# Optimization experiments

Hardware: AMD Instinct MI355X
Metric: run time of the kernel (lower is better)

The kernel has to match this reference:

```python
import jax, jax.numpy as jnp
import numpy as np

N, E, D, L, G = 50000, 625000, 128, 3, 64
EPS = 1e-5


def setup_inputs() -> dict:
    key = jax.random.key(0)
    ks = jax.random.split(key, 16)
    s = 1.0 / np.sqrt(D)
    inp = {
        "x": jax.random.normal(ks[0], (N, D), jnp.float32),
        "edge_index": jax.random.randint(ks[1], (2, E), 0, N, jnp.int64),
        "batch": jnp.sort(jax.random.randint(ks[2], (N,), 0, G, jnp.int64)),
        # node_emb
        "Wemb": jax.random.normal(ks[3], (D, D), jnp.float32) * s,
        "bemb": jnp.zeros((D,), jnp.float32),
        # per-layer params stacked on axis 0
        "Wscore": jax.random.normal(ks[4], (L, 1, D), jnp.float32) * s,
        "bscore": jnp.zeros((L, 1), jnp.float32),
        "Wfwd": jax.random.normal(ks[5], (L, D, D), jnp.float32) * s,
        "Wbwd": jax.random.normal(ks[6], (L, D, D), jnp.float32) * s,
        "Wself": jax.random.normal(ks[7], (L, D, D), jnp.float32) * s,
        "bself": jnp.zeros((L, D), jnp.float32),
        "Wcomb": jax.random.normal(ks[8], (L, D, 3 * D), jnp.float32) * s,
        "bcomb": jnp.zeros((L, D), jnp.float32),
        "gamma": jnp.ones((L, D), jnp.float32),
        "beta": jnp.zeros((L, D), jnp.float32),
    }
    return inp


def reference(x, edge_index, batch, Wemb, bemb, Wscore, bscore, Wfwd, Wbwd,
              Wself, bself, Wcomb, bcomb, gamma, beta):
    n = x.shape[0]
    src, dst = edge_index[0], edge_index[1]  # j (source), i (target)
    h = jax.nn.relu(x @ Wemb.T + bemb)       # dropout is eval-mode no-op
    for l in range(Wscore.shape[0]):
        identity = h
        scores = h @ Wscore[l].T + bscore[l]           # [N, 1]
        h_fwd = h @ Wfwd[l].T                          # [N, D]
        h_bwd = h @ Wbwd[l].T
        h_self = h @ Wself[l].T + bself[l]
        alpha = jax.nn.sigmoid(scores[src] - scores[dst])  # [E, 1]
        aggr_fwd = jax.ops.segment_sum(h_fwd[src] * alpha, dst, num_segments=n)
        aggr_bwd = jax.ops.segment_sum(h_bwd[src] * (1.0 - alpha), dst, num_segments=n)
        z = jnp.concatenate([h_self, aggr_fwd, aggr_bwd], axis=-1) @ Wcomb[l].T + bcomb[l]
        mu = jnp.mean(z, axis=-1, keepdims=True)
        var = jnp.var(z, axis=-1, keepdims=True)
        z = (z - mu) * jax.lax.rsqrt(var + EPS) * gamma[l] + beta[l]
        h = jax.nn.relu(z) + identity
    # global mean pool over graphs
    sums = jax.ops.segment_sum(h, batch, num_segments=G)
    cnt = jax.ops.segment_sum(jnp.ones((n,), h.dtype), batch, num_segments=G)
    return sums / jnp.maximum(cnt, 1.0)[:, None]
```

## Files before the change

### kernel.cpp

```cpp
#include <hip/hip_runtime.h>
#include <math.h>

#define EPS 1e-5f
#define PS 8
#define SW(row) (((row) & 7) << 4)

typedef __attribute__((ext_vector_type(8))) short short8;
typedef __attribute__((ext_vector_type(4))) float f32x4;

__device__ __forceinline__ float bf2f(unsigned short u) {
  union { unsigned i; float f; } c; c.i = ((unsigned)u) << 16; return c.f;
}
__device__ __forceinline__ float bflo(unsigned u) {
  union { unsigned i; float f; } c; c.i = u << 16; return c.f;
}
__device__ __forceinline__ float bfhi(unsigned u) {
  union { unsigned i; float f; } c; c.i = u & 0xFFFF0000u; return c.f;
}
__device__ __forceinline__ unsigned short f2bf(float f) {
  union { float f; unsigned i; } c; c.f = f;
  unsigned r = c.i + 0x7FFF + ((c.i >> 16) & 1);
  return (unsigned short)(r >> 16);
}

template <bool SCORE>
__global__ __launch_bounds__(256, 2) void embed_gemm(
    const float* __restrict__ X,
    const ushort* __restrict__ W,
    const float* __restrict__ bias,
    const float* __restrict__ Wsc, const float* __restrict__ bsc,
    ushort* __restrict__ hb, float* __restrict__ scores, int M) {
  __shared__ __align__(16) ushort As[64 * 128];
  __shared__ __align__(16) ushort Ws[128 * 128];
  __shared__ float lds3[64][2];

  const int t = threadIdx.x;
  const int lane = t & 63;
  const int w = t >> 6;
  const int wm = w >> 1, wn = w & 1;
  const int m0 = blockIdx.x * 64;
  const int l15 = lane & 15, l16 = lane >> 4;

  short8 ar[4], wr_[8];
#pragma unroll
  for (int it = 0; it < 4; ++it) {
    int chunk = it * 256 + t;
    int row = chunk >> 4;
    int b16 = chunk & 15;
    int grow = m0 + row; if (grow >= M) grow = M - 1;
    const float* xr = X + (size_t)grow * 128 + b16 * 8;
    float4 f0 = *(const float4*)xr;
    float4 f1 = *(const float4*)(xr + 4);
    short8 v;
    v[0] = (short)f2bf(f0.x); v[1] = (short)f2bf(f0.y);
    v[2] = (short)f2bf(f0.z); v[3] = (short)f2bf(f0.w);
    v[4] = (short)f2bf(f1.x); v[5] = (short)f2bf(f1.y);
    v[6] = (short)f2bf(f1.z); v[7] = (short)f2bf(f1.w);
    ar[it] = v;
  }
#pragma unroll
  for (int it = 0; it < 8; ++it) {
    int chunk = it * 256 + t;
    int row = chunk >> 4;
    int b16 = chunk & 15;
    wr_[it] = *(const short8*)(W + (size_t)row * 128 + b16 * 8);
  }
#pragma unroll
  for (int it = 0; it < 4; ++it) {
    int chunk = it * 256 + t;
    int row = chunk >> 4, b = (chunk & 15) * 16;
    *(short8*)((char*)As + row * 256 + (b ^ SW(row))) = ar[it];
  }
#pragma unroll
  for (int it = 0; it < 8; ++it) {
    int chunk = it * 256 + t;
    int row = chunk >> 4, b = (chunk & 15) * 16;
    *(short8*)((char*)Ws + row * 256 + (b ^ SW(row))) = wr_[it];
  }
  __syncthreads();

  f32x4 acc[2][4];
#pragma unroll
  for (int i = 0; i < 2; ++i)
#pragma unroll
    for (int j = 0; j < 4; ++j) acc[i][j] = (f32x4){0.f, 0.f, 0.f, 0.f};

#pragma unroll
  for (int kk = 0; kk < 4; ++kk) {
    int cb = kk * 64 + l16 * 16;
    short8 a[2], b[4];
#pragma unroll
    for (int i = 0; i < 2; ++i) {
      int row = wm * 32 + i * 16 + l15;
      a[i] = *(const short8*)((const char*)As + row * 256 + (cb ^ SW(row)));
    }
#pragma unroll
    for (int j = 0; j < 4; ++j) {
      int row = wn * 64 + j * 16 + l15;
      b[j] = *(const short8*)((const char*)Ws + row * 256 + (cb ^ SW(row)));
    }
#pragma unroll
    for (int i = 0; i < 2; ++i)
#pragma unroll
      for (int j = 0; j < 4; ++j)
        acc[i][j] = __builtin_amdgcn_mfma_f32_16x16x32_bf16(a[i], b[j], acc[i][j], 0, 0, 0);
  }

#pragma unroll
  for (int i = 0; i < 2; ++i)
#pragma unroll
    for (int r = 0; r < 4; ++r) {
      int row = m0 + wm * 32 + i * 16 + l16 * 4 + r;
      bool valid = row < M;
      float psc = 0.f;
#pragma unroll
      for (int j = 0; j < 4; ++j) {
        int colw = wn * 64 + j * 16 + l15;
        float v = acc[i][j][r] + bias[colw];
        v = fmaxf(v, 0.f);
        if (valid) hb[(size_t)row * 128 + colw] = f2bf(v);
        if (SCORE) psc += v * Wsc[colw];
      }
      if (SCORE) {
#pragma unroll
        for (int mm = 1; mm <= 8; mm <<= 1) psc += __shfl_xor(psc, mm, 64);
        if (l15 == 0) lds3[wm * 32 + i * 16 + l16 * 4 + r][wn] = psc;
      }
    }
  if (SCORE) {
    __syncthreads();
    if (wn == 0 && l15 == 0) {
#pragma unroll
      for (int i = 0; i < 2; ++i)
#pragma unroll
        for (int r = 0; r < 4; ++r) {
          int rl = wm * 32 + i * 16 + l16 * 4 + r;
          int row = blockIdx.x * 64 + rl;
          if (row < M) scores[row] = lds3[rl][0] + lds3[rl][1] + bsc[0];
        }
    }
  }
}

template <bool SCORE>
__global__ __launch_bounds__(256, 2) void layer_gemm(
    const ushort* __restrict__ A0,
    const ushort* __restrict__ A1,
    const ushort* __restrict__ W,
    const float* __restrict__ bias,
    const float* __restrict__ gamma, const float* __restrict__ beta,
    const float* __restrict__ Wsc, const float* __restrict__ bsc,
    ushort* __restrict__ hb, float* __restrict__ scores, int M) {
  __shared__ __align__(16) ushort As[64 * 192];
  __shared__ __align__(16) ushort Ws[128 * 192];
  __shared__ float lds1[64][2];
  __shared__ float lds2[64][2];
  __shared__ float lds3[64][2];

  const int t = threadIdx.x;
  const int lane = t & 63;
  const int w = t >> 6;
  const int wm = w >> 1, wn = w & 1;
  const int m0 = blockIdx.x * 64;
  const int l15 = lane & 15, l16 = lane >> 4;

  f32x4 acc[2][4];
#pragma unroll
  for (int i = 0; i < 2; ++i)
#pragma unroll
    for (int j = 0; j < 4; ++j) acc[i][j] = (f32x4){0.f, 0.f, 0.f, 0.f};

#pragma unroll
  for (int hf = 0; hf < 2; ++hf) {
    short8 ar[6], wr_[12];
#pragma unroll
    for (int it = 0; it < 6; ++it) {
      int chunk = it * 256 + t;
      int row = chunk / 24;
      int b16 = chunk % 24;
      int ec = hf * 192 + b16 * 8;
      int grow = m0 + row; if (grow >= M) grow = M - 1;
      const ushort* src = (ec < 128) ? (A0 + (size_t)grow * 128 + ec)
                                     : (A1 + (size_t)grow * 256 + (ec - 128));
      ar[it] = *(const short8*)src;
    }
#pragma unroll
    for (int it = 0; it < 12; ++it) {
      int chunk = it * 256 + t;
      int row = chunk / 24;
      int b16 = chunk % 24;
      wr_[it] = *(const short8*)(W + (size_t)row * 384 + hf * 192 + b16 * 8);
    }
    __syncthreads();
#pragma unroll
    for (int it = 0; it < 6; ++it) {
      int chunk = it * 256 + t;
      int row = chunk / 24, b = (chunk % 24) * 16;
      *(short8*)((char*)As + row * 384 + (b ^ SW(row))) = ar[it];
    }
#pragma unroll
    for (int it = 0; it < 12; ++it) {
      int chunk = it * 256 + t;
      int row = chunk / 24, b = (chunk % 24) * 16;
      *(short8*)((char*)Ws + row * 384 + (b ^ SW(row))) = wr_[it];
    }
    __syncthreads();
#pragma unroll
    for (int kk = 0; kk < 6; ++kk) {
      int cb = kk * 64 + l16 * 16;
      short8 a[2], b[4];
#pragma unroll
      for (int i = 0; i < 2; ++i) {
        int row = wm * 32 + i * 16 + l15;
        a[i] = *(const short8*)((const char*)As + row * 384 + (cb ^ SW(row)));
      }
#pragma unroll
      for (int j = 0; j < 4; ++j) {
        int row = wn * 64 + j * 16 + l15;
        b[j] = *(const short8*)((const char*)Ws + row * 384 + (cb ^ SW(row)));
      }
#pragma unroll
      for (int i = 0; i < 2; ++i)
#pragma unroll
        for (int j = 0; j < 4; ++j)
          acc[i][j] = __builtin_amdgcn_mfma_f32_16x16x32_bf16(a[i], b[j], acc[i][j], 0, 0, 0);
    }
  }

#pragma unroll
  for (int i = 0; i < 2; ++i)
#pragma unroll
    for (int r = 0; r < 4; ++r) {
      float p1 = 0.f, p2 = 0.f;
#pragma unroll
      for (int j = 0; j < 4; ++j) {
        int colw = wn * 64 + j * 16 + l15;
        float v = acc[i][j][r] + bias[colw];
        acc[i][j][r] = v;
        p1 += v;
        p2 += v * v;
      }
#pragma unroll
      for (int mm = 1; mm <= 8; mm <<= 1) {
        p1 += __shfl_xor(p1, mm, 64);
        p2 += __shfl_xor(p2, mm, 64);
      }
      if (l15 == 0) {
        int rl = wm * 32 + i * 16 + l16 * 4 + r;
        lds1[rl][wn] = p1;
        lds2[rl][wn] = p2;
      }
    }
  __syncthreads();
#pragma unroll
  for (int i = 0; i < 2; ++i)
#pragma unroll
    for (int r = 0; r < 4; ++r) {
      int rl = wm * 32 + i * 16 + l16 * 4 + r;
      int row = m0 + rl;
      bool valid = row < M;
      float s1 = lds1[rl][0] + lds1[rl][1];
      float s2 = lds2[rl][0] + lds2[rl][1];
      float mu = s1 * (1.f / 128.f);
      float var = s2 * (1.f / 128.f) - mu * mu;
      float rs = rsqrtf(var + EPS);
      float psc = 0.f;
#pragma unroll
      for (int j = 0; j < 4; ++j) {
        int colw = wn * 64 + j * 16 + l15;
        float v = acc[i][j][r];
        float o = (v - mu) * rs * gamma[colw] + beta[colw];
        o = fmaxf(o, 0.f);
        float res = o;
        if (valid) {
          res = o + bf2f(hb[(size_t)row * 128 + colw]);
          hb[(size_t)row * 128 + colw] = f2bf(res);
        }
        if (SCORE) psc += res * Wsc[colw];
      }
      if (SCORE) {
#pragma unroll
        for (int mm = 1; mm <= 8; mm <<= 1) psc += __shfl_xor(psc, mm, 64);
        if (l15 == 0) lds3[rl][wn] = psc;
      }
    }
  if (SCORE) {
    __syncthreads();
    if (wn == 0 && l15 == 0) {
#pragma unroll
      for (int i = 0; i < 2; ++i)
#pragma unroll
        for (int r = 0; r < 4; ++r) {
          int rl = wm * 32 + i * 16 + l16 * 4 + r;
          int row = m0 + rl;
          if (row < M) scores[row] = lds3[rl][0] + lds3[rl][1] + bsc[0];
        }
    }
  }
}

__global__ __launch_bounds__(256) void wpre_kernel(
    const float* __restrict__ Wcomb, const float* __restrict__ Wself,
    const float* __restrict__ Wfwd, const float* __restrict__ Wbwd,
    ushort* __restrict__ Wbig) {
  const int l = blockIdx.x / 3, p = blockIdx.x % 3;
  const float* Wc = Wcomb + (size_t)l * 128 * 384;
  const float* Wp = (p == 0 ? Wself : (p == 1 ? Wfwd : Wbwd)) + (size_t)l * 128 * 128;
  __shared__ float Bs[128][132];
  const int t = threadIdx.x;
  for (int i = t; i < 16384; i += 256) Bs[i >> 7][i & 127] = Wp[i];
  __syncthreads();
  const int r = t >> 1;
  const int c0 = (t & 1) * 64;
  float acc[64];
#pragma unroll
  for (int c = 0; c < 64; ++c) acc[c] = 0.f;
  for (int k = 0; k < 128; ++k) {
    float a = Wc[(size_t)r * 384 + p * 128 + k];
#pragma unroll
    for (int c4 = 0; c4 < 16; ++c4) {
      float4 b4 = *(const float4*)&Bs[k][c0 + c4 * 4];
      acc[c4 * 4 + 0] = fmaf(a, b4.x, acc[c4 * 4 + 0]);
      acc[c4 * 4 + 1] = fmaf(a, b4.y, acc[c4 * 4 + 1]);
      acc[c4 * 4 + 2] = fmaf(a, b4.z, acc[c4 * 4 + 2]);
      acc[c4 * 4 + 3] = fmaf(a, b4.w, acc[c4 * 4 + 3]);
    }
  }
  ushort* o = Wbig + (size_t)l * 128 * 384 + (size_t)r * 384 + p * 128 + c0;
#pragma unroll
  for (int c = 0; c < 64; ++c) o[c] = f2bf(acc[c]);
}

__global__ void bpre_kernel(const float* __restrict__ Wcomb, const float* __restrict__ bself,
                            const float* __restrict__ bcomb, float* __restrict__ biasc, int L) {
  int idx = blockIdx.x * 128 + threadIdx.x;
  if (idx >= L * 128) return;
  int l = idx >> 7;
  const float* Wc = Wcomb + (size_t)l * 128 * 384 + (size_t)(idx & 127) * 384;
  const float* bs = bself + (size_t)l * 128;
  float acc = bcomb[idx];
  for (int k = 0; k < 128; ++k) acc = fmaf(Wc[k], bs[k], acc);
  biasc[idx] = acc;
}

__global__ void f2b_kernel(const float* __restrict__ in, ushort* __restrict__ out, int n4) {
  int i = blockIdx.x * 256 + threadIdx.x;
  if (i < n4) {
    float4 v = ((const float4*)in)[i];
    ushort4 o;
    o.x = f2bf(v.x); o.y = f2bf(v.y); o.z = f2bf(v.z); o.w = f2bf(v.w);
    ((ushort4*)out)[i] = o;
  }
}

__global__ void hist_kernel(const int* __restrict__ dst, int* __restrict__ counts, int E) {
  int e = blockIdx.x * 256 + threadIdx.x;
  if (e < E) atomicAdd(&counts[dst[e]], 1);
}

__global__ __launch_bounds__(256) void scan1_kernel(
    const int* __restrict__ c, int* __restrict__ ex, int* __restrict__ partials, int n) {
  __shared__ int sd[256];
  int t = threadIdx.x, b = blockIdx.x;
  int base = b * 1024 + t * 4;
  int v0 = (base + 0 < n) ? c[base + 0] : 0;
  int v1 = (base + 1 < n) ? c[base + 1] : 0;
  int v2 = (base + 2 < n) ? c[base + 2] : 0;
  int v3 = (base + 3 < n) ? c[base + 3] : 0;
  int tot = v0 + v1 + v2 + v3;
  sd[t] = tot;
  __syncthreads();
  for (int off = 1; off < 256; off <<= 1) {
    int x = (t >= off) ? sd[t - off] : 0;
    __syncthreads();
    sd[t] += x;
    __syncthreads();
  }
  int p = sd[t] - tot;
  if (base + 0 < n) ex[base + 0] = p;
  if (base + 1 < n) ex[base + 1] = p + v0;
  if (base + 2 < n) ex[base + 2] = p + v0 + v1;
  if (base + 3 < n) ex[base + 3] = p + v0 + v1 + v2;
  if (t == 255) partials[b] = sd[255];
}

__global__ __launch_bounds__(256) void scan2_kernel(int* __restrict__ partials, int nb) {
  __shared__ int sd[256];
  int t = threadIdx.x;
  int v = (t < nb) ? partials[t] : 0;
  sd[t] = v;
  __syncthreads();
  for (int off = 1; off < 256; off <<= 1) {
    int x = (t >= off) ? sd[t - off] : 0;
    __syncthreads();
    sd[t] += x;
    __syncthreads();
  }
  if (t < nb) partials[t] = sd[t] - v;
}

__global__ void scan3_kernel(const int* __restrict__ ex, const int* __restrict__ partials,
                             int* __restrict__ indptr, int* __restrict__ cursor,
                             int n, int E) {
  int i = blockIdx.x * 256 + threadIdx.x;
  if (i < n) {
    int v = ex[i] + partials[i >> 10];
    indptr[i] = v;
    cursor[i] = v;
  }
  if (i == 0) indptr[n] = E;
}

__global__ void scatter_kernel(const int* __restrict__ ei, int* __restrict__ cursor,
                               int* __restrict__ ssrc, int E) {
  int e = blockIdx.x * 256 + threadIdx.x;
  if (e >= E) return;
  int s = ei[e];
  int d = ei[E + e];
  int pos = atomicAdd(&cursor[d], 1);
  ssrc[pos] = s;
}

__global__ __launch_bounds__(256) void aggr_kernel(
    const int* __restrict__ indptr, const int* __restrict__ ssrc,
    const float* __restrict__ scores, const ushort* __restrict__ hb,
    ushort* __restrict__ uv, int Nn) {
  const int t = threadIdx.x;
  const int lane = t & 63;
  const int q = lane & 15;
  const int qbase = lane & 48;
  const int node = blockIdx.x * 16 + (t >> 6) * 4 + (lane >> 4);
  if (node >= Nn) return;
  int beg = indptr[node], end = indptr[node + 1];
  float si = scores[node];
  float u0 = 0.f, u1 = 0.f, u2 = 0.f, u3 = 0.f;
  float u4 = 0.f, u5 = 0.f, u6 = 0.f, u7 = 0.f;
  float t0 = 0.f, t1 = 0.f, t2 = 0.f, t3 = 0.f;
  float t4 = 0.f, t5 = 0.f, t6 = 0.f, t7 = 0.f;

  for (int ebase = beg; ebase < end; ebase += 16) {
    int cnt = min(16, end - ebase);
    int sv = 0;
    float al = 0.f;
    if (q < cnt) {
      sv = ssrc[ebase + q];
      al = 1.f / (1.f + __expf(si - scores[sv]));
    }
    int e = 0;
    for (; e + 4 <= cnt; e += 4) {
      int s0 = __shfl(sv, qbase + e, 64),     s1 = __shfl(sv, qbase + e + 1, 64);
      int s2 = __shfl(sv, qbase + e + 2, 64), s3 = __shfl(sv, qbase + e + 3, 64);
      float a0 = __shfl(al, qbase + e, 64),     a1 = __shfl(al, qbase + e + 1, 64);
      float a2 = __shfl(al, qbase + e + 2, 64), a3 = __shfl(al, qbase + e + 3, 64);
      uint4 v0 = *(const uint4*)(hb + (size_t)s0 * 128 + q * 8);
      uint4 v1 = *(const uint4*)(hb + (size_t)s1 * 128 + q * 8);
      uint4 v2 = *(const uint4*)(hb + (size_t)s2 * 128 + q * 8);
      uint4 v3 = *(const uint4*)(hb + (size_t)s3 * 128 + q * 8);
      float f;
#define ACC8(V, A)                                              \
      f = bflo(V.x); u0 = fmaf(A, f, u0); t0 += f;              \
      f = bfhi(V.x); u1 = fmaf(A, f, u1); t1 += f;              \
      f = bflo(V.y); u2 = fmaf(A, f, u2); t2 += f;              \
      f = bfhi(V.y); u3 = fmaf(A, f, u3); t3 += f;              \
      f = bflo(V.z); u4 = fmaf(A, f, u4); t4 += f;              \
      f = bfhi(V.z); u5 = fmaf(A, f, u5); t5 += f;              \
      f = bflo(V.w); u6 = fmaf(A, f, u6); t6 += f;              \
      f = bfhi(V.w); u7 = fmaf(A, f, u7); t7 += f;
      ACC8(v0, a0)
      ACC8(v1, a1)
      ACC8(v2, a2)
      ACC8(v3, a3)
    }
    for (; e < cnt; ++e) {
      int s_e = __shfl(sv, qbase + e, 64);
      float a_e = __shfl(al, qbase + e, 64);
      uint4 vv = *(const uint4*)(hb + (size_t)s_e * 128 + q * 8);
      float f;
      ACC8(vv, a_e)
#undef ACC8
    }
  }
  uint4 pu, pv;
  pu.x = (unsigned)f2bf(u0) | ((unsigned)f2bf(u1) << 16);
  pu.y = (unsigned)f2bf(u2) | ((unsigned)f2bf(u3) << 16);
  pu.z = (unsigned)f2bf(u4) | ((unsigned)f2bf(u5) << 16);
  pu.w = (unsigned)f2bf(u6) | ((unsigned)f2bf(u7) << 16);
  pv.x = (unsigned)f2bf(t0 - u0) | ((unsigned)f2bf(t1 - u1) << 16);
  pv.y = (unsigned)f2bf(t2 - u2) | ((unsigned)f2bf(t3 - u3) << 16);
  pv.z = (unsigned)f2bf(t4 - u4) | ((unsigned)f2bf(t5 - u5) << 16);
  pv.w = (unsigned)f2bf(t6 - u6) | ((unsigned)f2bf(t7 - u7) << 16);
  *(uint4*)(uv + (size_t)node * 256 + q * 8) = pu;
  *(uint4*)(uv + (size_t)node * 256 + 128 + q * 8) = pv;
}

__global__ __launch_bounds__(128) void pool_stage_kernel(
    const ushort* __restrict__ hb, const int* __restrict__ batch,
    float* __restrict__ partial, int M) {
  int g = blockIdx.x, s = blockIdx.y, d = threadIdx.x;
  int lo = 0, hi = M;
  while (lo < hi) { int mid = (lo + hi) >> 1; if (batch[mid] < g) lo = mid + 1; else hi = mid; }
  int b0 = lo;
  hi = M;
  while (lo < hi) { int mid = (lo + hi) >> 1; if (batch[mid] <= g) lo = mid + 1; else hi = mid; }
  int b1 = lo;
  int len = b1 - b0;
  int chunk = (len + PS - 1) / PS;
  int r0 = b0 + s * chunk;
  int r1 = min(b1, r0 + chunk);
  float acc = 0.f;
  for (int i = r0; i < r1; ++i) acc += bf2f(hb[(size_t)i * 128 + d]);
  partial[((size_t)g * PS + s) * 128 + d] = acc;
}

__global__ void pool_final_kernel(const float* __restrict__ partial,
                                  const int* __restrict__ batch,
                                  float* __restrict__ out, int M, int G) {
  int idx = blockIdx.x * 256 + threadIdx.x;
  if (idx >= G * 128) return;
  int g = idx >> 7, d = idx & 127;
  float acc = 0.f;
#pragma unroll
  for (int s = 0; s < PS; ++s) acc += partial[((size_t)g * PS + s) * 128 + d];
  int lo = 0, hi = M;
  while (lo < hi) { int mid = (lo + hi) >> 1; if (batch[mid] < g) lo = mid + 1; else hi = mid; }
  int b0 = lo;
  hi = M;
  while (lo < hi) { int mid = (lo + hi) >> 1; if (batch[mid] <= g) lo = mid + 1; else hi = mid; }
  int c = lo - b0;
  out[idx] = acc / (float)(c > 0 ? c : 1);
}

extern "C" void kernel_launch(void* const* d_in, const int* in_sizes, int n_in,
                              void* d_out, int out_size, void* d_ws, size_t ws_size,
                              hipStream_t stream) {
  const float* x      = (const float*)d_in[0];
  const int*   ei     = (const int*)d_in[1];
  const int*   batch  = (const int*)d_in[2];
  const float* Wemb   = (const float*)d_in[3];
  const float* bemb   = (const float*)d_in[4];
  const float* Wscore = (const float*)d_in[5];
  const float* bscore = (const float*)d_in[6];
  const float* Wfwd   = (const float*)d_in[7];
  const float* Wbwd   = (const float*)d_in[8];
  const float* Wself  = (const float*)d_in[9];
  const float* bself  = (const float*)d_in[10];
  const float* Wcomb  = (const float*)d_in[11];
  const float* bcomb  = (const float*)d_in[12];
  const float* gamma  = (const float*)d_in[13];
  const float* beta   = (const float*)d_in[14];

  const int N = in_sizes[0] / 128;
  const int E = in_sizes[1] / 2;
  const int L = in_sizes[5] / 128;
  const int G = out_size / 128;
  float* out = (float*)d_out;

  char* p = (char*)d_ws;
  auto alloc = [&](size_t bytes) -> char* {
    char* r = p;
    p += (bytes + 255) & ~(size_t)255;
    return r;
  };
  ushort* hb16   = (ushort*)alloc((size_t)N * 128 * 2);
  ushort* uv     = (ushort*)alloc((size_t)N * 256 * 2);
  float*  scores = (float*)alloc((size_t)N * 4);
  ushort* Wemb_b = (ushort*)alloc(16384 * 2);
  ushort* Wbig   = (ushort*)alloc((size_t)L * 128 * 384 * 2);
  float*  biasc  = (float*)alloc((size_t)L * 128 * 4);
  int* counts    = (int*)alloc((size_t)N * 4);
  int* ex        = (int*)alloc((size_t)N * 4);
  int* partials  = (int*)alloc(1024);
  int* indptr    = (int*)alloc((size_t)(N + 1) * 4);
  int* cursor    = (int*)alloc((size_t)N * 4);
  int* ssrc      = (int*)alloc((size_t)E * 4);
  float* pool_p  = (float*)alloc((size_t)G * PS * 128 * 4);

  const int gb = (N + 63) / 64;

  f2b_kernel<<<16, 256, 0, stream>>>(Wemb, Wemb_b, 4096);
  wpre_kernel<<<3 * L, 256, 0, stream>>>(Wcomb, Wself, Wfwd, Wbwd, Wbig);
  bpre_kernel<<<L, 128, 0, stream>>>(Wcomb, bself, bcomb, biasc, L);

  hipMemsetAsync(counts, 0, (size_t)N * 4, stream);
  hist_kernel<<<(E + 255) / 256, 256, 0, stream>>>(ei + E, counts, E);
  int nb = (N + 1023) / 1024;
  scan1_kernel<<<nb, 256, 0, stream>>>(counts, ex, partials, N);
  scan2_kernel<<<1, 256, 0, stream>>>(partials, nb);
  scan3_kernel<<<(N + 255) / 256, 256, 0, stream>>>(ex, partials, indptr, cursor, N, E);
  scatter_kernel<<<(E + 255) / 256, 256, 0, stream>>>(ei, cursor, ssrc, E);

  embed_gemm<true><<<gb, 256, 0, stream>>>(x, Wemb_b, bemb, Wscore, bscore,
                                           hb16, scores, N);

  for (int l = 0; l < L; ++l) {
    aggr_kernel<<<(N + 15) / 16, 256, 0, stream>>>(indptr, ssrc, scores, hb16, uv, N);
    if (l < L - 1) {
      layer_gemm<true><<<gb, 256, 0, stream>>>(
          hb16, uv, Wbig + (size_t)l * 128 * 384, biasc + (size_t)l * 128,
          gamma + (size_t)l * 128, beta + (size_t)l * 128,
          Wscore + (size_t)(l + 1) * 128, bscore + (l + 1), hb16, scores, N);
    } else {
      layer_gemm<false><<<gb, 256, 0, stream>>>(
          hb16, uv, Wbig + (size_t)l * 128 * 384, biasc + (size_t)l * 128,
          gamma + (size_t)l * 128, beta + (size_t)l * 128,
          nullptr, nullptr, hb16, scores, N);
    }
  }

  pool_stage_kernel<<<dim3(G, PS), 128, 0, stream>>>(hb16, batch, pool_p, N);
  pool_final_kernel<<<(G * 128 + 255) / 256, 256, 0, stream>>>(pool_p, batch, out, N, G);
}
```

Before: 425.4 us.

## Fuse edge aggregation into the per-layer GEMM kernel with ping-pong buffers

The separate aggregation kernel is folded into the layer GEMM. Each block gathers neighbor features for its 64 rows and writes the forward and backward aggregates straight into shared memory, so the uv intermediate no longer round-trips through global memory. The GEMM now streams weights in six 64-wide K slices, and node features and scores are double-buffered across layers to avoid read/write hazards. The tradeoff is that the irregular gather runs inside a GEMM block limited by launch bounds, which may reduce latency hiding compared with the standalone aggregation kernel.

```diff
diff --git a/kernel.cpp b/kernel.cpp
--- a/kernel.cpp
+++ b/kernel.cpp
@@ -143,26 +143,116 @@
 }
 
 template <bool SCORE>
-__global__ __launch_bounds__(256, 2) void layer_gemm(
-    const ushort* __restrict__ A0,
-    const ushort* __restrict__ A1,
+__global__ __launch_bounds__(256, 2) void fused_layer(
+    const int* __restrict__ indptr, const int* __restrict__ ssrc,
+    const float* __restrict__ sc_in, const ushort* __restrict__ hin,
     const ushort* __restrict__ W,
     const float* __restrict__ bias,
     const float* __restrict__ gamma, const float* __restrict__ beta,
     const float* __restrict__ Wsc, const float* __restrict__ bsc,
-    ushort* __restrict__ hb, float* __restrict__ scores, int M) {
-  __shared__ __align__(16) ushort As[64 * 192];
-  __shared__ __align__(16) ushort Ws[128 * 192];
+    ushort* __restrict__ hout, float* __restrict__ sc_out, int M) {
+  __shared__ __align__(16) ushort As_h[64 * 128];
+  __shared__ __align__(16) ushort As_u[64 * 128];
+  __shared__ __align__(16) ushort As_v[64 * 128];
+  __shared__ __align__(16) ushort Ws_[128 * 64];
   __shared__ float lds1[64][2];
   __shared__ float lds2[64][2];
   __shared__ float lds3[64][2];
 
   const int t = threadIdx.x;
   const int lane = t & 63;
-  const int w = t >> 6;
-  const int wm = w >> 1, wn = w & 1;
+  const int w4 = t >> 6;
+  const int wm = w4 >> 1, wn = w4 & 1;
   const int m0 = blockIdx.x * 64;
   const int l15 = lane & 15, l16 = lane >> 4;
+  const int q = lane & 15;
+  const int qbase = lane & 48;
+  const int qsel = lane >> 4;
+
+#pragma unroll 1
+  for (int round = 0; round < 4; ++round) {
+    int rl = w4 * 16 + round * 4 + qsel;
+    int node = m0 + rl;
+    int beg = 0, end = 0;
+    float si = 0.f;
+    if (node < M) { beg = indptr[node]; end = indptr[node + 1]; si = sc_in[node]; }
+    float u0 = 0.f, u1 = 0.f, u2 = 0.f, u3 = 0.f;
+    float u4 = 0.f, u5 = 0.f, u6 = 0.f, u7 = 0.f;
+    float t0 = 0.f, t1 = 0.f, t2 = 0.f, t3 = 0.f;
+    float t4 = 0.f, t5 = 0.f, t6 = 0.f, t7 = 0.f;
+    for (int ebase = beg; ebase < end; ebase += 16) {
+      int cnt = min(16, end - ebase);
+      int sv = 0;
+      float al = 0.f;
+      if (q < cnt) {
+        sv = ssrc[ebase + q];
+        al = 1.f / (1.f + __expf(si - sc_in[sv]));
+      }
+      int e = 0;
+      for (; e + 4 <= cnt; e += 4) {
+        int s0 = __shfl(sv, qbase + e, 64),     s1 = __shfl(sv, qbase + e + 1, 64);
+        int s2 = __shfl(sv, qbase + e + 2, 64), s3 = __shfl(sv, qbase + e + 3, 64);
+        float a0 = __shfl(al, qbase + e, 64),     a1 = __shfl(al, qbase + e + 1, 64);
+        float a2 = __shfl(al, qbase + e + 2, 64), a3 = __shfl(al, qbase + e + 3, 64);
+        uint4 v0 = *(const uint4*)(hin + (size_t)s0 * 128 + q * 8);
+        uint4 v1 = *(const uint4*)(hin + (size_t)s1 * 128 + q * 8);
+        uint4 v2 = *(const uint4*)(hin + (size_t)s2 * 128 + q * 8);
+        uint4 v3 = *(const uint4*)(hin + (size_t)s3 * 128 + q * 8);
+        float f;
+#define ACC8(V, A)                                              \
+        f = bflo(V.x); u0 = fmaf(A, f, u0); t0 += f;            \
+        f = bfhi(V.x); u1 = fmaf(A, f, u1); t1 += f;            \
+        f = bflo(V.y); u2 = fmaf(A, f, u2); t2 += f;            \
+        f = bfhi(V.y); u3 = fmaf(A, f, u3); t3 += f;            \
+        f = bflo(V.z); u4 = fmaf(A, f, u4); t4 += f;            \
+        f = bfhi(V.z); u5 = fmaf(A, f, u5); t5 += f;            \
+        f = bflo(V.w); u6 = fmaf(A, f, u6); t6 += f;            \
+        f = bfhi(V.w); u7 = fmaf(A, f, u7); t7 += f;
+        ACC8(v0, a0)
+        ACC8(v1, a1)
+        ACC8(v2, a2)
+        ACC8(v3, a3)
+      }
+      for (; e < cnt; ++e) {
+        int s_e = __shfl(sv, qbase + e, 64);
+        float a_e = __shfl(al, qbase + e, 64);
+        uint4 vv = *(const uint4*)(hin + (size_t)s_e * 128 + q * 8);
+        float f;
+        ACC8(vv, a_e)
+#undef ACC8
+      }
+    }
+    short8 pu, pv;
+    pu[0] = (short)f2bf(u0); pu[1] = (short)f2bf(u1);
+    pu[2] = (short)f2bf(u2); pu[3] = (short)f2bf(u3);
+    pu[4] = (short)f2bf(u4); pu[5] = (short)f2bf(u5);
+    pu[6] = (short)f2bf(u6); pu[7] = (short)f2bf(u7);
+    pv[0] = (short)f2bf(t0 - u0); pv[1] = (short)f2bf(t1 - u1);
+    pv[2] = (short)f2bf(t2 - u2); pv[3] = (short)f2bf(t3 - u3);
+    pv[4] = (short)f2bf(t4 - u4); pv[5] = (short)f2bf(t5 - u5);
+    pv[6] = (short)f2bf(t6 - u6); pv[7] = (short)f2bf(t7 - u7);
+    *(short8*)((char*)As_u + rl * 256 + ((q * 16) ^ SW(rl))) = pu;
+    *(short8*)((char*)As_v + rl * 256 + ((q * 16) ^ SW(rl))) = pv;
+  }
+
+  {
+    short8 ar[4];
+#pragma unroll
+    for (int it = 0; it < 4; ++it) {
+      int chunk = it * 256 + t;
+      int row = chunk >> 4;
+      int b16 = chunk & 15;
+      int grow = m0 + row; if (grow >= M) grow = M - 1;
+      ar[it] = *(const short8*)(hin + (size_t)grow * 128 + b16 * 8);
+    }
+#pragma unroll
+    for (int it = 0; it < 4; ++it) {
+      int chunk = it * 256 + t;
+      int row = chunk >> 4, b = (chunk & 15) * 16;
+      *(short8*)((char*)As_h + row * 256 + (b ^ SW(row))) = ar[it];
+    }
+  }
+  __syncthreads();
 
   f32x4 acc[2][4];
 #pragma unroll
@@ -170,54 +260,39 @@
 #pragma unroll
     for (int j = 0; j < 4; ++j) acc[i][j] = (f32x4){0.f, 0.f, 0.f, 0.f};
 
-#pragma unroll
-  for (int hf = 0; hf < 2; ++hf) {
-    short8 ar[6], wr_[12];
-#pragma unroll
-    for (int it = 0; it < 6; ++it) {
+#pragma unroll 1
+  for (int s = 0; s < 6; ++s) {
+    short8 wr_[4];
+#pragma unroll
+    for (int it = 0; it < 4; ++it) {
       int chunk = it * 256 + t;
-      int row = chunk / 24;
-      int b16 = chunk % 24;
-      int ec = hf * 192 + b16 * 8;
-      int grow = m0 + row; if (grow >= M) grow = M - 1;
-      const ushort* src = (ec < 128) ? (A0 + (size_t)grow * 128 + ec)
-                                     : (A1 + (size_t)grow * 256 + (ec - 128));
-      ar[it] = *(const short8*)src;
-    }
-#pragma unroll
-    for (int it = 0; it < 12; ++it) {
+      int row = chunk >> 3;
+      int c8 = chunk & 7;
+      wr_[it] = *(const short8*)(W + (size_t)row * 384 + s * 64 + c8 * 8);
+    }
+    __syncthreads();
+#pragma unroll
+    for (int it = 0; it < 4; ++it) {
       int chunk = it * 256 + t;
-      int row = chunk / 24;
-      int b16 = chunk % 24;
-      wr_[it] = *(const short8*)(W + (size_t)row * 384 + hf * 192 + b16 * 8);
-    }
-    __syncthreads();
-#pragma unroll
-    for (int it = 0; it < 6; ++it) {
-      int chunk = it * 256 + t;
-      int row = chunk / 24, b = (chunk % 24) * 16;
-      *(short8*)((char*)As + row * 384 + (b ^ SW(row))) = ar[it];
-    }
-#pragma unroll
-    for (int it = 0; it < 12; ++it) {
-      int chunk = it * 256 + t;
-      int row = chunk / 24, b = (chunk % 24) * 16;
-      *(short8*)((char*)Ws + row * 384 + (b ^ SW(row))) = wr_[it];
-    }
-    __syncthreads();
-#pragma unroll
-    for (int kk = 0; kk < 6; ++kk) {
-      int cb = kk * 64 + l16 * 16;
+      int row = chunk >> 3, b = (chunk & 7) * 16;
+      *(short8*)((char*)Ws_ + row * 128 + (b ^ SW(row))) = wr_[it];
+    }
+    __syncthreads();
+    const ushort* Asrc = (s < 2) ? As_h : (s < 4) ? As_u : As_v;
+#pragma unroll
+    for (int kk2 = 0; kk2 < 2; ++kk2) {
+      int cbA = (s & 1) * 128 + kk2 * 64 + l16 * 16;
+      int cbW = kk2 * 64 + l16 * 16;
       short8 a[2], b[4];
 #pragma unroll
       for (int i = 0; i < 2; ++i) {
         int row = wm * 32 + i * 16 + l15;
-        a[i] = *(const short8*)((const char*)As + row * 384 + (cb ^ SW(row)));
+        a[i] = *(const short8*)((const char*)Asrc + row * 256 + (cbA ^ SW(row)));
       }
 #pragma unroll
       for (int j = 0; j < 4; ++j) {
         int row = wn * 64 + j * 16 + l15;
-        b[j] = *(const short8*)((const char*)Ws + row * 384 + (cb ^ SW(row)));
+        b[j] = *(const short8*)((const char*)Ws_ + row * 128 + (cbW ^ SW(row)));
       }
 #pragma unroll
       for (int i = 0; i < 2; ++i)
@@ -273,8 +348,8 @@
         o = fmaxf(o, 0.f);
         float res = o;
         if (valid) {
-          res = o + bf2f(hb[(size_t)row * 128 + colw]);
-          hb[(size_t)row * 128 + colw] = f2bf(res);
+          res = o + bf2f(hin[(size_t)row * 128 + colw]);
+          hout[(size_t)row * 128 + colw] = f2bf(res);
         }
         if (SCORE) psc += res * Wsc[colw];
       }
@@ -293,7 +368,7 @@
         for (int r = 0; r < 4; ++r) {
           int rl = wm * 32 + i * 16 + l16 * 4 + r;
           int row = m0 + rl;
-          if (row < M) scores[row] = lds3[rl][0] + lds3[rl][1] + bsc[0];
+          if (row < M) sc_out[row] = lds3[rl][0] + lds3[rl][1] + bsc[0];
         }
     }
   }
@@ -419,78 +494,6 @@
   int d = ei[E + e];
   int pos = atomicAdd(&cursor[d], 1);
   ssrc[pos] = s;
-}
-
-__global__ __launch_bounds__(256) void aggr_kernel(
-    const int* __restrict__ indptr, const int* __restrict__ ssrc,
-    const float* __restrict__ scores, const ushort* __restrict__ hb,
-    ushort* __restrict__ uv, int Nn) {
-  const int t = threadIdx.x;
-  const int lane = t & 63;
-  const int q = lane & 15;
-  const int qbase = lane & 48;
-  const int node = blockIdx.x * 16 + (t >> 6) * 4 + (lane >> 4);
-  if (node >= Nn) return;
-  int beg = indptr[node], end = indptr[node + 1];
-  float si = scores[node];
-  float u0 = 0.f, u1 = 0.f, u2 = 0.f, u3 = 0.f;
-  float u4 = 0.f, u5 = 0.f, u6 = 0.f, u7 = 0.f;
-  float t0 = 0.f, t1 = 0.f, t2 = 0.f, t3 = 0.f;
-  float t4 = 0.f, t5 = 0.f, t6 = 0.f, t7 = 0.f;
-
-  for (int ebase = beg; ebase < end; ebase += 16) {
-    int cnt = min(16, end - ebase);
-    int sv = 0;
-    float al = 0.f;
-    if (q < cnt) {
-      sv = ssrc[ebase + q];
-      al = 1.f / (1.f + __expf(si - scores[sv]));
-    }
-    int e = 0;
-    for (; e + 4 <= cnt; e += 4) {
-      int s0 = __shfl(sv, qbase + e, 64),     s1 = __shfl(sv, qbase + e + 1, 64);
-      int s2 = __shfl(sv, qbase + e + 2, 64), s3 = __shfl(sv, qbase + e + 3, 64);
-      float a0 = __shfl(al, qbase + e, 64),     a1 = __shfl(al, qbase + e + 1, 64);
-      float a2 = __shfl(al, qbase + e + 2, 64), a3 = __shfl(al, qbase + e + 3, 64);
-      uint4 v0 = *(const uint4*)(hb + (size_t)s0 * 128 + q * 8);
-      uint4 v1 = *(const uint4*)(hb + (size_t)s1 * 128 + q * 8);
-      uint4 v2 = *(const uint4*)(hb + (size_t)s2 * 128 + q * 8);
-      uint4 v3 = *(const uint4*)(hb + (size_t)s3 * 128 + q * 8);
-      float f;
-#define ACC8(V, A)                                              \
-      f = bflo(V.x); u0 = fmaf(A, f, u0); t0 += f;              \
-      f = bfhi(V.x); u1 = fmaf(A, f, u1); t1 += f;              \
-      f = bflo(V.y); u2 = fmaf(A, f, u2); t2 += f;              \
-      f = bfhi(V.y); u3 = fmaf(A, f, u3); t3 += f;              \
-      f = bflo(V.z); u4 = fmaf(A, f, u4); t4 += f;              \
-      f = bfhi(V.z); u5 = fmaf(A, f, u5); t5 += f;              \
-      f = bflo(V.w); u6 = fmaf(A, f, u6); t6 += f;              \
-      f = bfhi(V.w); u7 = fmaf(A, f, u7); t7 += f;
-      ACC8(v0, a0)
-      ACC8(v1, a1)
-      ACC8(v2, a2)
-      ACC8(v3, a3)
-    }
-    for (; e < cnt; ++e) {
-      int s_e = __shfl(sv, qbase + e, 64);
-      float a_e = __shfl(al, qbase + e, 64);
-      uint4 vv = *(const uint4*)(hb + (size_t)s_e * 128 + q * 8);
-      float f;
-      ACC8(vv, a_e)
-#undef ACC8
-    }
-  }
-  uint4 pu, pv;
-  pu.x = (unsigned)f2bf(u0) | ((unsigned)f2bf(u1) << 16);
-  pu.y = (unsigned)f2bf(u2) | ((unsigned)f2bf(u3) << 16);
-  pu.z = (unsigned)f2bf(u4) | ((unsigned)f2bf(u5) << 16);
-  pu.w = (unsigned)f2bf(u6) | ((unsigned)f2bf(u7) << 16);
-  pv.x = (unsigned)f2bf(t0 - u0) | ((unsigned)f2bf(t1 - u1) << 16);
-  pv.y = (unsigned)f2bf(t2 - u2) | ((unsigned)f2bf(t3 - u3) << 16);
-  pv.z = (unsigned)f2bf(t4 - u4) | ((unsigned)f2bf(t5 - u5) << 16);
-  pv.w = (unsigned)f2bf(t6 - u6) | ((unsigned)f2bf(t7 - u7) << 16);
-  *(uint4*)(uv + (size_t)node * 256 + q * 8) = pu;
-  *(uint4*)(uv + (size_t)node * 256 + 128 + q * 8) = pv;
 }
 
 __global__ __launch_bounds__(128) void pool_stage_kernel(
@@ -561,9 +564,10 @@
     p += (bytes + 255) & ~(size_t)255;
     return r;
   };
-  ushort* hb16   = (ushort*)alloc((size_t)N * 128 * 2);
-  ushort* uv     = (ushort*)alloc((size_t)N * 256 * 2);
-  float*  scores = (float*)alloc((size_t)N * 4);
+  ushort* hb0    = (ushort*)alloc((size_t)N * 128 * 2);
+  ushort* hb1    = (ushort*)alloc((size_t)N * 128 * 2);
+  float*  sc0    = (float*)alloc((size_t)N * 4);
+  float*  sc1    = (float*)alloc((size_t)N * 4);
   ushort* Wemb_b = (ushort*)alloc(16384 * 2);
   ushort* Wbig   = (ushort*)alloc((size_t)L * 128 * 384 * 2);
   float*  biasc  = (float*)alloc((size_t)L * 128 * 4);
@@ -575,6 +579,9 @@
   int* ssrc      = (int*)alloc((size_t)E * 4);
   float* pool_p  = (float*)alloc((size_t)G * PS * 128 * 4);
 
+  ushort* hbuf[2] = { hb0, hb1 };
+  float*  sbuf[2] = { sc0, sc1 };
+
   const int gb = (N + 63) / 64;
 
   f2b_kernel<<<16, 256, 0, stream>>>(Wemb, Wemb_b, 4096);
@@ -590,23 +597,26 @@
   scatter_kernel<<<(E + 255) / 256, 256, 0, stream>>>(ei, cursor, ssrc, E);
 
   embed_gemm<true><<<gb, 256, 0, stream>>>(x, Wemb_b, bemb, Wscore, bscore,
-                                           hb16, scores, N);
+                                           hbuf[0], sbuf[0], N);
 
   for (int l = 0; l < L; ++l) {
-    aggr_kernel<<<(N + 15) / 16, 256, 0, stream>>>(indptr, ssrc, scores, hb16, uv, N);
+    int in = l & 1, ot = (l + 1) & 1;
     if (l < L - 1) {
-      layer_gemm<true><<<gb, 256, 0, stream>>>(
-          hb16, uv, Wbig + (size_t)l * 128 * 384, biasc + (size_t)l * 128,
+      fused_layer<true><<<gb, 256, 0, stream>>>(
+          indptr, ssrc, sbuf[in], hbuf[in],
+          Wbig + (size_t)l * 128 * 384, biasc + (size_t)l * 128,
           gamma + (size_t)l * 128, beta + (size_t)l * 128,
-          Wscore + (size_t)(l + 1) * 128, bscore + (l + 1), hb16, scores, N);
+          Wscore + (size_t)(l + 1) * 128, bscore + (l + 1),
+          hbuf[ot], sbuf[ot], N);
     } else {
-      layer_gemm<false><<<gb, 256, 0, stream>>>(
-          hb16, uv, Wbig + (size_t)l * 128 * 384, biasc + (size_t)l * 128,
+      fused_layer<false><<<gb, 256, 0, stream>>>(
+          indptr, ssrc, sbuf[in], hbuf[in],
+          Wbig + (size_t)l * 128 * 384, biasc + (size_t)l * 128,
           gamma + (size_t)l * 128, beta + (size_t)l * 128,
-          nullptr, nullptr, hb16, scores, N);
-    }
-  }
-
-  pool_stage_kernel<<<dim3(G, PS), 128, 0, stream>>>(hb16, batch, pool_p, N);
+          nullptr, nullptr, hbuf[ot], sbuf[ot], N);
+    }
+  }
+
+  pool_stage_kernel<<<dim3(G, PS), 128, 0, stream>>>(hbuf[L & 1], batch, pool_p, N);
   pool_final_kernel<<<(G * 128 + 255) / 256, 256, 0, stream>>>(pool_p, batch, out, N, G);
 }
```

Measured after the change: 463.0 us. 8.8% more time.
